# Optimization experiments

Hardware: AMD Instinct MI355X
Metric: run time of the kernel (lower is better)

Reference implementation:

```python
import jax, jax.numpy as jnp
import numpy as np

EPS = 1e-5

def _rmsnorm(x, eps=1e-6):
    # non-affine RMSNorm over last dim (BitNet SubLN-style pre-quant norm)
    return x * jax.lax.rsqrt(jnp.mean(x * x, axis=-1, keepdims=True) + eps)

def _act_quant(x):
    # per-token int8 absmax quantization
    scale = 127.0 / jnp.clip(jnp.max(jnp.abs(x), axis=-1, keepdims=True), EPS)
    return jnp.clip(jnp.round(x * scale), -128, 127) / scale

def _weight_quant(w):
    # per-tensor ternary (1.58-bit) quantization
    scale = 1.0 / jnp.clip(jnp.mean(jnp.abs(w)), EPS)
    return jnp.clip(jnp.round(w * scale), -1, 1) / scale

def _ste(a, q):
    # straight-through estimator: forward = q, backward grad flows to a
    return a + jax.lax.stop_gradient(q - a)

def _bitlinear(x, w):
    # x: [..., in_features], w: [out_features, in_features], no bias
    xn = _rmsnorm(x)
    xq = _ste(xn, _act_quant(xn))
    wq = _ste(w, _weight_quant(w))
    return jnp.einsum('bsd,hd->bsh', xq, wq)


def setup_inputs() -> dict:
    key = jax.random.key(0)
    k_x, k1, k2, k3 = jax.random.split(key, 4)
    B, S, D, H = 4, 4096, 2048, 5632  # hidden = 256*ceil(2048*8/3 / 256)
    return {
        'x': jax.random.normal(k_x, (B, S, D), dtype=jnp.float32),
        'w1': jax.random.normal(k1, (H, D), dtype=jnp.float32) * 0.02,
        'w2': jax.random.normal(k2, (H, D), dtype=jnp.float32) * 0.02,
        'w3': jax.random.normal(k3, (D, H), dtype=jnp.float32) * 0.02,
    }


def reference(x, w1, w2, w3):
    gate = jax.nn.silu(_bitlinear(x, w1))
    up = _bitlinear(x, w2)
    return _bitlinear(gate * up, w3)
```

## Files before the change

kernel.cpp:

```cpp
#include <hip/hip_runtime.h>

typedef int i32x4 __attribute__((ext_vector_type(4)));

static constexpr int M_TOK = 16384;
static constexpr int D_IN  = 2048;
static constexpr int H_FF  = 5632;
static constexpr int NW    = H_FF * D_IN;

__device__ __forceinline__ void async16(const void* g, void* l) {
    __builtin_amdgcn_global_load_lds((__attribute__((address_space(1))) void*)g,
                                     (__attribute__((address_space(3))) void*)l,
                                     16, 0, 0);
}

__device__ __forceinline__ void sbar() {
    asm volatile("" ::: "memory");
    __builtin_amdgcn_s_barrier();
    asm volatile("" ::: "memory");
}
#define WAIT_LGKM(n) { asm volatile("s_waitcnt lgkmcnt(" #n ")" ::: "memory"); \
                       __builtin_amdgcn_sched_barrier(0); }
#define WAIT_VM(n)   { asm volatile("s_waitcnt vmcnt(" #n ")" ::: "memory"); }

__global__ void absum_partial(const float4* __restrict__ w, int n4, double* __restrict__ part) {
    __shared__ double s[256];
    const int t = threadIdx.x;
    double acc = 0.0;
    for (int i = blockIdx.x * 256 + t; i < n4; i += gridDim.x * 256) {
        float4 v = w[i];
        acc += fabs((double)v.x) + fabs((double)v.y) + fabs((double)v.z) + fabs((double)v.w);
    }
    s[t] = acc;
    __syncthreads();
    for (int o = 128; o > 0; o >>= 1) {
        if (t < o) s[t] += s[t + o];
        __syncthreads();
    }
    if (t == 0) part[blockIdx.x] = s[0];
}

__global__ void finalize_scales(const double* __restrict__ parts, double* __restrict__ scales,
                                int nblocks, double inv_n) {
    const int t = threadIdx.x;
    if (t < 3) {
        const double* p = parts + t * nblocks;
        double s = 0.0;
        for (int i = 0; i < nblocks; ++i) s += p[i];
        double c = fmax(s * inv_n, 1e-5);
        scales[t * 2]     = 1.0 / c;
        scales[t * 2 + 1] = c;
    }
}

__global__ void quant_w_kernel(const float4* __restrict__ w, unsigned int* __restrict__ tw,
                               const double* __restrict__ scales, int idx, int n4) {
    const double s = scales[idx * 2];
    const int stride = gridDim.x * blockDim.x;
    for (int i = blockIdx.x * blockDim.x + threadIdx.x; i < n4; i += stride) {
        float4 v = w[i];
        int q0 = (int)fmin(fmax(rint((double)v.x * s), -1.0), 1.0);
        int q1 = (int)fmin(fmax(rint((double)v.y * s), -1.0), 1.0);
        int q2 = (int)fmin(fmax(rint((double)v.z * s), -1.0), 1.0);
        int q3 = (int)fmin(fmax(rint((double)v.w * s), -1.0), 1.0);
        tw[i] = (unsigned int)((q0 & 255) | ((q1 & 255) << 8) |
                               ((q2 & 255) << 16) | ((q3 & 255) << 24));
    }
}

__global__ void quant_x_kernel(const float* __restrict__ x, signed char* __restrict__ qx,
                               double* __restrict__ cx) {
    __shared__ double ssum[256];
    __shared__ float  smax[256];
    const int token = blockIdx.x;
    const int t = threadIdx.x;
    const float4* xr = (const float4*)(x + (size_t)token * D_IN);
    float4 v0 = xr[t];
    float4 v1 = xr[t + 256];
    double ss = (double)v0.x*v0.x + (double)v0.y*v0.y + (double)v0.z*v0.z + (double)v0.w*v0.w
              + (double)v1.x*v1.x + (double)v1.y*v1.y + (double)v1.z*v1.z + (double)v1.w*v1.w;
    float mx = fmaxf(fmaxf(fmaxf(fabsf(v0.x), fabsf(v0.y)), fmaxf(fabsf(v0.z), fabsf(v0.w))),
                     fmaxf(fmaxf(fabsf(v1.x), fabsf(v1.y)), fmaxf(fabsf(v1.z), fabsf(v1.w))));
    ssum[t] = ss; smax[t] = mx;
    __syncthreads();
    for (int o = 128; o > 0; o >>= 1) {
        if (t < o) { ssum[t] += ssum[t + o]; smax[t] = fmaxf(smax[t], smax[t + o]); }
        __syncthreads();
    }
    const double ms    = ssum[0] * (1.0 / (double)D_IN);
    const double r     = 1.0 / sqrt(ms + 1e-6);
    const double den   = fmax((double)smax[0] * r, 1e-5);
    const double scale = 127.0 / den;
    if (t == 0) cx[token] = den * (1.0 / 127.0);

    int q0 = (int)fmin(fmax(rint(((double)v0.x * r) * scale), -128.0), 127.0);
    int q1 = (int)fmin(fmax(rint(((double)v0.y * r) * scale), -128.0), 127.0);
    int q2 = (int)fmin(fmax(rint(((double)v0.z * r) * scale), -128.0), 127.0);
    int q3 = (int)fmin(fmax(rint(((double)v0.w * r) * scale), -128.0), 127.0);
    int q4 = (int)fmin(fmax(rint(((double)v1.x * r) * scale), -128.0), 127.0);
    int q5 = (int)fmin(fmax(rint(((double)v1.y * r) * scale), -128.0), 127.0);
    int q6 = (int)fmin(fmax(rint(((double)v1.z * r) * scale), -128.0), 127.0);
    int q7 = (int)fmin(fmax(rint(((double)v1.w * r) * scale), -128.0), 127.0);
    unsigned int* qr = (unsigned int*)(qx + (size_t)token * D_IN);
    qr[t]       = (unsigned int)((q0 & 255) | ((q1 & 255) << 8) | ((q2 & 255) << 16) | ((q3 & 255) << 24));
    qr[t + 256] = (unsigned int)((q4 & 255) | ((q5 & 255) << 8) | ((q6 & 255) << 16) | ((q7 & 255) << 24));
}

__global__ void quant_h_kernel(float* __restrict__ h, double* __restrict__ ch) {
    __shared__ double ssum[256];
    __shared__ float  smax[256];
    const int token = blockIdx.x;
    const int t = threadIdx.x;
    float* hr = h + (size_t)token * H_FF;
    const float2* h2 = (const float2*)hr;
    float2 vals[11];
    double ss = 0.0;
    float mx = 0.f;
#pragma unroll
    for (int k = 0; k < 11; ++k) {
        float2 v = h2[t + 256 * k];
        vals[k] = v;
        ss += (double)v.x * (double)v.x + (double)v.y * (double)v.y;
        mx = fmaxf(mx, fmaxf(fabsf(v.x), fabsf(v.y)));
    }
    ssum[t] = ss; smax[t] = mx;
    __syncthreads();
    for (int o = 128; o > 0; o >>= 1) {
        if (t < o) { ssum[t] += ssum[t + o]; smax[t] = fmaxf(smax[t], smax[t + o]); }
        __syncthreads();
    }
    const double ms    = ssum[0] * (1.0 / (double)H_FF);
    const double r     = 1.0 / sqrt(ms + 1e-6);
    const double den   = fmax((double)smax[0] * r, 1e-5);
    const double scale = 127.0 / den;
    if (t == 0) ch[token] = den * (1.0 / 127.0);
    unsigned short* qr = (unsigned short*)hr;
#pragma unroll
    for (int k = 0; k < 11; ++k) {
        int a = (int)fmin(fmax(rint(((double)vals[k].x * r) * scale), -128.0), 127.0);
        int b = (int)fmin(fmax(rint(((double)vals[k].y * r) * scale), -128.0), 127.0);
        qr[t + 256 * k] = (unsigned short)((a & 255) | ((b & 255) << 8));
    }
}


__global__ void __launch_bounds__(512, 2) gemm12_kernel(
    const signed char* __restrict__ qx,
    const signed char* __restrict__ tw1,
    const signed char* __restrict__ tw2,
    const double* __restrict__ cx,
    const double* __restrict__ scales,
    float* __restrict__ h)
{
    __shared__ __attribute__((aligned(16))) signed char lds[4][32768];

    const int t = threadIdx.x;
    const int swz = (blockIdx.x & 7) * 352 + (blockIdx.x >> 3);
    const int bm  = swz & 63;
    const int bn  = swz >> 6;

    const int srow = t >> 2;
    const int scol = (((t & 3) ^ ((t >> 3) & 3)) << 4);
    const signed char* gA  = qx  + (size_t)(bm * 256 + srow) * D_IN + scol;
    const signed char* gB1 = tw1 + (size_t)(bn * 128 + srow) * D_IN + scol;
    const signed char* gB2 = tw2 + (size_t)(bn * 128 + srow) * D_IN + scol;
    const size_t arstep = (size_t)128 * D_IN;
    const int l16 = t * 16;

    const int lane = t & 63;
    const int wv = t >> 6;
    const int wm = wv & 3;
    const int wn = wv >> 2;
    const int lm = lane & 15;
    const int kg = lane >> 4;
    const int koff = ((kg ^ ((lm >> 1) & 3)) << 4);

    int aoff[4], boff[4];
#pragma unroll
    for (int i = 0; i < 4; ++i) aoff[i] = (wm * 64 + i * 16 + lm) * 64 + koff;
#pragma unroll
    for (int j = 0; j < 4; ++j) boff[j] = (wn * 64 + j * 16 + lm) * 64 + koff;

    const i32x4 izero = {0, 0, 0, 0};
    i32x4 acc1[4][4], acc2[4][4];
#pragma unroll
    for (int i = 0; i < 4; ++i)
#pragma unroll
        for (int j = 0; j < 4; ++j) { acc1[i][j] = izero; acc2[i][j] = izero; }

    constexpr int NT = D_IN / 64;

#define STAGE12(buf, kt) { const int go = (kt) * 64;                         \
        async16(gA + go,          &lds[buf][l16]);                           \
        async16(gA + arstep + go, &lds[buf][l16 + 8192]);                    \
        async16(gB1 + go, &lds[buf][16384 + l16]);                           \
        async16(gB2 + go, &lds[buf][24576 + l16]); }

    STAGE12(0, 0); STAGE12(1, 1); STAGE12(2, 2);
    WAIT_VM(8);
    sbar();

    for (int kt = 0; kt < NT; ++kt) {
        const int cur = kt & 3;

        i32x4 a[4], b1[4], b2[4];
#pragma unroll
        for (int i = 0; i < 4; ++i) a[i] = *(const i32x4*)&lds[cur][aoff[i]];
#pragma unroll
        for (int j = 0; j < 4; ++j) b1[j] = *(const i32x4*)&lds[cur][16384 + boff[j]];
        __builtin_amdgcn_sched_barrier(0);
#pragma unroll
        for (int j = 0; j < 4; ++j) b2[j] = *(const i32x4*)&lds[cur][24576 + boff[j]];
        __builtin_amdgcn_sched_barrier(0);
        if (kt + 3 < NT) STAGE12((kt + 3) & 3, kt + 3);

        WAIT_LGKM(4);
        __builtin_amdgcn_s_setprio(1);
#pragma unroll
        for (int i = 0; i < 4; ++i)
#pragma unroll
            for (int j = 0; j < 4; ++j)
                acc1[i][j] = __builtin_amdgcn_mfma_i32_16x16x64_i8(a[i], b1[j], acc1[i][j], 0, 0, 0);
        __builtin_amdgcn_s_setprio(0);
        WAIT_LGKM(0);
        __builtin_amdgcn_s_setprio(1);
#pragma unroll
        for (int i = 0; i < 4; ++i)
#pragma unroll
            for (int j = 0; j < 4; ++j)
                acc2[i][j] = __builtin_amdgcn_mfma_i32_16x16x64_i8(a[i], b2[j], acc2[i][j], 0, 0, 0);
        __builtin_amdgcn_s_setprio(0);

        if (kt + 3 < NT)      { WAIT_VM(8); }
        else if (kt + 2 < NT) { WAIT_VM(4); }
        else if (kt + 1 < NT) { WAIT_VM(0); }
        sbar();
    }
#undef STAGE12

    const double cw1 = scales[1];
    const double cw2 = scales[3];
#pragma unroll
    for (int i = 0; i < 4; ++i) {
#pragma unroll
        for (int v = 0; v < 4; ++v) {
            const int row = bm * 256 + wm * 64 + i * 16 + kg * 4 + v;
            const double c  = cx[row];
            const double s1 = c * cw1, s2 = c * cw2;
            float* hp = h + (size_t)row * H_FF + bn * 128 + wn * 64 + lm;
#pragma unroll
            for (int j = 0; j < 4; ++j) {
                float g  = (float)((double)acc1[i][j][v] * s1);
                float u  = (float)((double)acc2[i][j][v] * s2);
                float sg = g / (1.0f + expf(-g));
                hp[j * 16] = sg * u;
            }
        }
    }
}

__global__ void __launch_bounds__(512, 2) gemm3_kernel(
    const signed char* __restrict__ qh,
    const signed char* __restrict__ tw3,
    const double* __restrict__ ch,
    const double* __restrict__ scales,
    float* __restrict__ out)
{
    __shared__ __attribute__((aligned(16))) signed char lds[4][32768];

    const int t = threadIdx.x;
    const int swz = (blockIdx.x & 7) * 64 + (blockIdx.x >> 3);
    const int bm  = swz & 63;
    const int bn  = swz >> 6;

    const int srow = t >> 2;
    const int scol = (((t & 3) ^ ((t >> 3) & 3)) << 4);
    const size_t qh_stride = (size_t)4 * H_FF;
    const signed char* gA = qh  + (size_t)(bm * 256 + srow) * qh_stride + scol;
    const signed char* gB = tw3 + (size_t)(bn * 256 + srow) * H_FF + scol;
    const size_t arstep = (size_t)128 * qh_stride;
    const size_t brstep = (size_t)128 * H_FF;
    const int l16 = t * 16;

    const int lane = t & 63;
    const int wv = t >> 6;
    const int wm = wv >> 2;
    const int wn = wv & 3;
    const int lm = lane & 15;
    const int kg = lane >> 4;
    const int koff = ((kg ^ ((lm >> 1) & 3)) << 4);

    int aoff[8], boff[4];
#pragma unroll
    for (int i = 0; i < 8; ++i) aoff[i] = (wm * 128 + i * 16 + lm) * 64 + koff;
#pragma unroll
    for (int j = 0; j < 4; ++j) boff[j] = (wn * 64 + j * 16 + lm) * 64 + koff;

    const i32x4 izero = {0, 0, 0, 0};
    i32x4 acc[8][4];
#pragma unroll
    for (int i = 0; i < 8; ++i)
#pragma unroll
        for (int j = 0; j < 4; ++j) acc[i][j] = izero;

    constexpr int NT = H_FF / 64;

#define STAGE3(buf, kt) { const int go = (kt) * 64;                          \
        async16(gA + go,          &lds[buf][l16]);                           \
        async16(gA + arstep + go, &lds[buf][l16 + 8192]);                    \
        async16(gB + go,          &lds[buf][16384 + l16]);                   \
        async16(gB + brstep + go, &lds[buf][24576 + l16]); }

    STAGE3(0, 0); STAGE3(1, 1); STAGE3(2, 2);
    WAIT_VM(8);
    sbar();

    for (int kt = 0; kt < NT; ++kt) {
        const int cur = kt & 3;

        i32x4 a[4], b[4], a2[4];
#pragma unroll
        for (int i = 0; i < 4; ++i) a[i] = *(const i32x4*)&lds[cur][aoff[i]];
#pragma unroll
        for (int j = 0; j < 4; ++j) b[j] = *(const i32x4*)&lds[cur][16384 + boff[j]];
        __builtin_amdgcn_sched_barrier(0);
#pragma unroll
        for (int i = 0; i < 4; ++i) a2[i] = *(const i32x4*)&lds[cur][aoff[i + 4]];
        __builtin_amdgcn_sched_barrier(0);
        if (kt + 3 < NT) STAGE3((kt + 3) & 3, kt + 3);

        WAIT_LGKM(4);
        __builtin_amdgcn_s_setprio(1);
#pragma unroll
        for (int i = 0; i < 4; ++i)
#pragma unroll
            for (int j = 0; j < 4; ++j)
                acc[i][j] = __builtin_amdgcn_mfma_i32_16x16x64_i8(a[i], b[j], acc[i][j], 0, 0, 0);
        __builtin_amdgcn_s_setprio(0);
        WAIT_LGKM(0);
        __builtin_amdgcn_s_setprio(1);
#pragma unroll
        for (int i = 0; i < 4; ++i)
#pragma unroll
            for (int j = 0; j < 4; ++j)
                acc[i + 4][j] = __builtin_amdgcn_mfma_i32_16x16x64_i8(a2[i], b[j], acc[i + 4][j], 0, 0, 0);
        __builtin_amdgcn_s_setprio(0);

        if (kt + 3 < NT)      { WAIT_VM(8); }
        else if (kt + 2 < NT) { WAIT_VM(4); }
        else if (kt + 1 < NT) { WAIT_VM(0); }
        sbar();
    }
#undef STAGE3

    const double cw3 = scales[5];
#pragma unroll
    for (int i = 0; i < 8; ++i) {
#pragma unroll
        for (int v = 0; v < 4; ++v) {
            const int row = bm * 256 + wm * 128 + i * 16 + kg * 4 + v;
            const double sc = ch[row] * cw3;
            float* op = out + (size_t)row * D_IN + bn * 256 + wn * 64 + lm;
#pragma unroll
            for (int j = 0; j < 4; ++j) op[j * 16] = (float)((double)acc[i][j][v] * sc);
        }
    }
}

extern "C" void kernel_launch(void* const* d_in, const int* in_sizes, int n_in,
                              void* d_out, int out_size, void* d_ws, size_t ws_size,
                              hipStream_t stream) {
    const float* x  = (const float*)d_in[0];
    const float* w1 = (const float*)d_in[1];
    const float* w2 = (const float*)d_in[2];
    const float* w3 = (const float*)d_in[3];

    char* ws = (char*)d_ws;
    double*      scales = (double*)(ws + 0);
    double*      parts  = (double*)(ws + 256);
    double*      cx     = (double*)(ws + 25088);
    double*      ch     = (double*)(ws + 156416);
    signed char* tw1    = (signed char*)(ws + 287744);
    signed char* tw2    = (signed char*)(ws + 11822336);
    signed char* tw3    = (signed char*)(ws + 23356928);
    float*       hb     = (float*)(ws + 34891520);
    signed char* qx     = (signed char*)(ws + 403990528);

    absum_partial<<<1024, 256, 0, stream>>>((const float4*)w1, NW / 4, parts);
    absum_partial<<<1024, 256, 0, stream>>>((const float4*)w2, NW / 4, parts + 1024);
    absum_partial<<<1024, 256, 0, stream>>>((const float4*)w3, NW / 4, parts + 2048);
    finalize_scales<<<1, 64, 0, stream>>>(parts, scales, 1024, 1.0 / (double)NW);
    quant_w_kernel<<<2048, 256, 0, stream>>>((const float4*)w1, (unsigned int*)tw1, scales, 0, NW / 4);
    quant_w_kernel<<<2048, 256, 0, stream>>>((const float4*)w2, (unsigned int*)tw2, scales, 1, NW / 4);
    quant_w_kernel<<<2048, 256, 0, stream>>>((const float4*)w3, (unsigned int*)tw3, scales, 2, NW / 4);
    quant_x_kernel<<<M_TOK, 256, 0, stream>>>(x, qx, cx);
    gemm12_kernel<<<2816, 512, 0, stream>>>(qx, tw1, tw2, cx, scales, hb);
    quant_h_kernel<<<M_TOK, 256, 0, stream>>>(hb, ch);
    gemm3_kernel<<<512, 512, 0, stream>>>((const signed char*)hb, tw3, ch, scales, (float*)d_out);
}
```

Baseline: 1.100 ms.

## Register double-buffer LDS fragments with 3-stage ring and remap block tile order

Both int8 GEMM kernels now prefetch the next K-tile's LDS fragments into a second register set while MFMAs run on the current set. The shared-memory ring drops from four stages to three, with one barrier per tile placed before staging. The block-to-tile mapping is changed from M-major to N-major grouping for L2 reuse. tw2 is now addressed as tw1+NW, with the workspace offsets moved so the two arrays are contiguous. This is meant to hide LDS read latency behind MFMA work, at the cost of extra VGPRs for the doubled fragment registers, which could hurt occupancy.

```diff
diff --git a/kernel.cpp b/kernel.cpp
--- a/kernel.cpp
+++ b/kernel.cpp
@@ -146,23 +146,21 @@
 __global__ void __launch_bounds__(512, 2) gemm12_kernel(
     const signed char* __restrict__ qx,
     const signed char* __restrict__ tw1,
-    const signed char* __restrict__ tw2,
     const double* __restrict__ cx,
     const double* __restrict__ scales,
     float* __restrict__ h)
 {
-    __shared__ __attribute__((aligned(16))) signed char lds[4][32768];
+    __shared__ __attribute__((aligned(16))) signed char lds[3][32768];
 
     const int t = threadIdx.x;
     const int swz = (blockIdx.x & 7) * 352 + (blockIdx.x >> 3);
-    const int bm  = swz & 63;
-    const int bn  = swz >> 6;
+    const int bm  = swz / 44;
+    const int bn  = swz % 44;
 
     const int srow = t >> 2;
     const int scol = (((t & 3) ^ ((t >> 3) & 3)) << 4);
     const signed char* gA  = qx  + (size_t)(bm * 256 + srow) * D_IN + scol;
     const signed char* gB1 = tw1 + (size_t)(bn * 128 + srow) * D_IN + scol;
-    const signed char* gB2 = tw2 + (size_t)(bn * 128 + srow) * D_IN + scol;
     const size_t arstep = (size_t)128 * D_IN;
     const int l16 = t * 16;
 
@@ -172,13 +170,9 @@
     const int wn = wv >> 2;
     const int lm = lane & 15;
     const int kg = lane >> 4;
-    const int koff = ((kg ^ ((lm >> 1) & 3)) << 4);
-
-    int aoff[4], boff[4];
-#pragma unroll
-    for (int i = 0; i < 4; ++i) aoff[i] = (wm * 64 + i * 16 + lm) * 64 + koff;
-#pragma unroll
-    for (int j = 0; j < 4; ++j) boff[j] = (wn * 64 + j * 16 + lm) * 64 + koff;
+    const int koff  = ((kg ^ ((lm >> 1) & 3)) << 4);
+    const int abase = (wm * 64 + lm) * 64 + koff;
+    const int bbase = (wn * 64 + lm) * 64 + koff;
 
     const i32x4 izero = {0, 0, 0, 0};
     i32x4 acc1[4][4], acc2[4][4];
@@ -187,55 +181,53 @@
 #pragma unroll
         for (int j = 0; j < 4; ++j) { acc1[i][j] = izero; acc2[i][j] = izero; }
 
+    i32x4 fA[12], fB[12];
+
     constexpr int NT = D_IN / 64;
 
 #define STAGE12(buf, kt) { const int go = (kt) * 64;                         \
-        async16(gA + go,          &lds[buf][l16]);                           \
-        async16(gA + arstep + go, &lds[buf][l16 + 8192]);                    \
-        async16(gB1 + go, &lds[buf][16384 + l16]);                           \
-        async16(gB2 + go, &lds[buf][24576 + l16]); }
+        async16(gA + go,           &lds[buf][l16]);                          \
+        async16(gA + arstep + go,  &lds[buf][l16 + 8192]);                   \
+        async16(gB1 + go,          &lds[buf][16384 + l16]);                  \
+        async16(gB1 + NW + go,     &lds[buf][24576 + l16]); }
+#define LOADF12(R, buf) {                                                    \
+        _Pragma("unroll") for (int i = 0; i < 4; ++i)                        \
+            R[i]     = *(const i32x4*)&lds[buf][abase + i * 1024];           \
+        _Pragma("unroll") for (int j = 0; j < 4; ++j)                        \
+            R[4 + j] = *(const i32x4*)&lds[buf][16384 + bbase + j * 1024];   \
+        _Pragma("unroll") for (int j = 0; j < 4; ++j)                        \
+            R[8 + j] = *(const i32x4*)&lds[buf][24576 + bbase + j * 1024]; }
+#define MFMAS12(R) {                                                         \
+        __builtin_amdgcn_s_setprio(1);                                       \
+        _Pragma("unroll") for (int i = 0; i < 4; ++i)                        \
+        _Pragma("unroll") for (int j = 0; j < 4; ++j)                        \
+            acc1[i][j] = __builtin_amdgcn_mfma_i32_16x16x64_i8(R[i], R[4 + j], acc1[i][j], 0, 0, 0); \
+        _Pragma("unroll") for (int i = 0; i < 4; ++i)                        \
+        _Pragma("unroll") for (int j = 0; j < 4; ++j)                        \
+            acc2[i][j] = __builtin_amdgcn_mfma_i32_16x16x64_i8(R[i], R[8 + j], acc2[i][j], 0, 0, 0); \
+        __builtin_amdgcn_s_setprio(0); }
+#define TILE12(kt, RCUR, RNXT) {                                             \
+        if ((kt) + 2 < NT) { WAIT_VM(4); } else { WAIT_VM(0); }              \
+        sbar();                                                              \
+        if ((kt) + 3 < NT) STAGE12(((kt) % 3), (kt) + 3);                    \
+        if ((kt) + 1 < NT) LOADF12(RNXT, (((kt) + 1) % 3));                  \
+        __builtin_amdgcn_sched_barrier(0);                                   \
+        MFMAS12(RCUR);                                                       \
+        WAIT_LGKM(0); }
 
     STAGE12(0, 0); STAGE12(1, 1); STAGE12(2, 2);
-    WAIT_VM(8);
-    sbar();
-
-    for (int kt = 0; kt < NT; ++kt) {
-        const int cur = kt & 3;
-
-        i32x4 a[4], b1[4], b2[4];
-#pragma unroll
-        for (int i = 0; i < 4; ++i) a[i] = *(const i32x4*)&lds[cur][aoff[i]];
-#pragma unroll
-        for (int j = 0; j < 4; ++j) b1[j] = *(const i32x4*)&lds[cur][16384 + boff[j]];
-        __builtin_amdgcn_sched_barrier(0);
-#pragma unroll
-        for (int j = 0; j < 4; ++j) b2[j] = *(const i32x4*)&lds[cur][24576 + boff[j]];
-        __builtin_amdgcn_sched_barrier(0);
-        if (kt + 3 < NT) STAGE12((kt + 3) & 3, kt + 3);
-
-        WAIT_LGKM(4);
-        __builtin_amdgcn_s_setprio(1);
-#pragma unroll
-        for (int i = 0; i < 4; ++i)
-#pragma unroll
-            for (int j = 0; j < 4; ++j)
-                acc1[i][j] = __builtin_amdgcn_mfma_i32_16x16x64_i8(a[i], b1[j], acc1[i][j], 0, 0, 0);
-        __builtin_amdgcn_s_setprio(0);
-        WAIT_LGKM(0);
-        __builtin_amdgcn_s_setprio(1);
-#pragma unroll
-        for (int i = 0; i < 4; ++i)
-#pragma unroll
-            for (int j = 0; j < 4; ++j)
-                acc2[i][j] = __builtin_amdgcn_mfma_i32_16x16x64_i8(a[i], b2[j], acc2[i][j], 0, 0, 0);
-        __builtin_amdgcn_s_setprio(0);
-
-        if (kt + 3 < NT)      { WAIT_VM(8); }
-        else if (kt + 2 < NT) { WAIT_VM(4); }
-        else if (kt + 1 < NT) { WAIT_VM(0); }
-        sbar();
+    WAIT_VM(8); sbar();
+    LOADF12(fA, 0);
+    WAIT_LGKM(0);
+
+    for (int kt = 0; kt < NT; kt += 2) {
+        TILE12(kt,     fA, fB);
+        TILE12(kt + 1, fB, fA);
     }
 #undef STAGE12
+#undef LOADF12
+#undef MFMAS12
+#undef TILE12
 
     const double cw1 = scales[1];
     const double cw2 = scales[3];
@@ -265,12 +257,12 @@
     const double* __restrict__ scales,
     float* __restrict__ out)
 {
-    __shared__ __attribute__((aligned(16))) signed char lds[4][32768];
+    __shared__ __attribute__((aligned(16))) signed char lds[3][32768];
 
     const int t = threadIdx.x;
     const int swz = (blockIdx.x & 7) * 64 + (blockIdx.x >> 3);
-    const int bm  = swz & 63;
-    const int bn  = swz >> 6;
+    const int bm  = swz >> 3;
+    const int bn  = swz & 7;
 
     const int srow = t >> 2;
     const int scol = (((t & 3) ^ ((t >> 3) & 3)) << 4);
@@ -287,13 +279,9 @@
     const int wn = wv & 3;
     const int lm = lane & 15;
     const int kg = lane >> 4;
-    const int koff = ((kg ^ ((lm >> 1) & 3)) << 4);
-
-    int aoff[8], boff[4];
-#pragma unroll
-    for (int i = 0; i < 8; ++i) aoff[i] = (wm * 128 + i * 16 + lm) * 64 + koff;
-#pragma unroll
-    for (int j = 0; j < 4; ++j) boff[j] = (wn * 64 + j * 16 + lm) * 64 + koff;
+    const int koff  = ((kg ^ ((lm >> 1) & 3)) << 4);
+    const int abase = (wm * 128 + lm) * 64 + koff;
+    const int bbase = (wn * 64 + lm) * 64 + koff;
 
     const i32x4 izero = {0, 0, 0, 0};
     i32x4 acc[8][4];
@@ -301,6 +289,8 @@
     for (int i = 0; i < 8; ++i)
 #pragma unroll
         for (int j = 0; j < 4; ++j) acc[i][j] = izero;
+
+    i32x4 fA[12], fB[12];
 
     constexpr int NT = H_FF / 64;
 
@@ -309,48 +299,44 @@
         async16(gA + arstep + go, &lds[buf][l16 + 8192]);                    \
         async16(gB + go,          &lds[buf][16384 + l16]);                   \
         async16(gB + brstep + go, &lds[buf][24576 + l16]); }
+#define LOADF3(R, buf) {                                                     \
+        _Pragma("unroll") for (int i = 0; i < 4; ++i)                        \
+            R[i]     = *(const i32x4*)&lds[buf][abase + i * 1024];           \
+        _Pragma("unroll") for (int j = 0; j < 4; ++j)                        \
+            R[4 + j] = *(const i32x4*)&lds[buf][16384 + bbase + j * 1024];   \
+        _Pragma("unroll") for (int i = 0; i < 4; ++i)                        \
+            R[8 + i] = *(const i32x4*)&lds[buf][abase + 4096 + i * 1024]; }
+#define MFMAS3(R) {                                                          \
+        __builtin_amdgcn_s_setprio(1);                                       \
+        _Pragma("unroll") for (int i = 0; i < 4; ++i)                        \
+        _Pragma("unroll") for (int j = 0; j < 4; ++j)                        \
+            acc[i][j] = __builtin_amdgcn_mfma_i32_16x16x64_i8(R[i], R[4 + j], acc[i][j], 0, 0, 0); \
+        _Pragma("unroll") for (int i = 0; i < 4; ++i)                        \
+        _Pragma("unroll") for (int j = 0; j < 4; ++j)                        \
+            acc[4 + i][j] = __builtin_amdgcn_mfma_i32_16x16x64_i8(R[8 + i], R[4 + j], acc[4 + i][j], 0, 0, 0); \
+        __builtin_amdgcn_s_setprio(0); }
+#define TILE3(kt, RCUR, RNXT) {                                              \
+        if ((kt) + 2 < NT) { WAIT_VM(4); } else { WAIT_VM(0); }              \
+        sbar();                                                              \
+        if ((kt) + 3 < NT) STAGE3(((kt) % 3), (kt) + 3);                     \
+        if ((kt) + 1 < NT) LOADF3(RNXT, (((kt) + 1) % 3));                   \
+        __builtin_amdgcn_sched_barrier(0);                                   \
+        MFMAS3(RCUR);                                                        \
+        WAIT_LGKM(0); }
 
     STAGE3(0, 0); STAGE3(1, 1); STAGE3(2, 2);
-    WAIT_VM(8);
-    sbar();
-
-    for (int kt = 0; kt < NT; ++kt) {
-        const int cur = kt & 3;
-
-        i32x4 a[4], b[4], a2[4];
-#pragma unroll
-        for (int i = 0; i < 4; ++i) a[i] = *(const i32x4*)&lds[cur][aoff[i]];
-#pragma unroll
-        for (int j = 0; j < 4; ++j) b[j] = *(const i32x4*)&lds[cur][16384 + boff[j]];
-        __builtin_amdgcn_sched_barrier(0);
-#pragma unroll
-        for (int i = 0; i < 4; ++i) a2[i] = *(const i32x4*)&lds[cur][aoff[i + 4]];
-        __builtin_amdgcn_sched_barrier(0);
-        if (kt + 3 < NT) STAGE3((kt + 3) & 3, kt + 3);
-
-        WAIT_LGKM(4);
-        __builtin_amdgcn_s_setprio(1);
-#pragma unroll
-        for (int i = 0; i < 4; ++i)
-#pragma unroll
-            for (int j = 0; j < 4; ++j)
-                acc[i][j] = __builtin_amdgcn_mfma_i32_16x16x64_i8(a[i], b[j], acc[i][j], 0, 0, 0);
-        __builtin_amdgcn_s_setprio(0);
-        WAIT_LGKM(0);
-        __builtin_amdgcn_s_setprio(1);
-#pragma unroll
-        for (int i = 0; i < 4; ++i)
-#pragma unroll
-            for (int j = 0; j < 4; ++j)
-                acc[i + 4][j] = __builtin_amdgcn_mfma_i32_16x16x64_i8(a2[i], b[j], acc[i + 4][j], 0, 0, 0);
-        __builtin_amdgcn_s_setprio(0);
-
-        if (kt + 3 < NT)      { WAIT_VM(8); }
-        else if (kt + 2 < NT) { WAIT_VM(4); }
-        else if (kt + 1 < NT) { WAIT_VM(0); }
-        sbar();
+    WAIT_VM(8); sbar();
+    LOADF3(fA, 0);
+    WAIT_LGKM(0);
+
+    for (int kt = 0; kt < NT; kt += 2) {
+        TILE3(kt,     fA, fB);
+        TILE3(kt + 1, fB, fA);
     }
 #undef STAGE3
+#undef LOADF3
+#undef MFMAS3
+#undef TILE3
 
     const double cw3 = scales[5];
 #pragma unroll
@@ -380,8 +366,8 @@
     double*      cx     = (double*)(ws + 25088);
     double*      ch     = (double*)(ws + 156416);
     signed char* tw1    = (signed char*)(ws + 287744);
-    signed char* tw2    = (signed char*)(ws + 11822336);
-    signed char* tw3    = (signed char*)(ws + 23356928);
+    signed char* tw2    = (signed char*)(ws + 11822080);
+    signed char* tw3    = (signed char*)(ws + 23356416);
     float*       hb     = (float*)(ws + 34891520);
     signed char* qx     = (signed char*)(ws + 403990528);
 
@@ -393,7 +379,7 @@
     quant_w_kernel<<<2048, 256, 0, stream>>>((const float4*)w2, (unsigned int*)tw2, scales, 1, NW / 4);
     quant_w_kernel<<<2048, 256, 0, stream>>>((const float4*)w3, (unsigned int*)tw3, scales, 2, NW / 4);
     quant_x_kernel<<<M_TOK, 256, 0, stream>>>(x, qx, cx);
-    gemm12_kernel<<<2816, 512, 0, stream>>>(qx, tw1, tw2, cx, scales, hb);
+    gemm12_kernel<<<2816, 512, 0, stream>>>(qx, tw1, cx, scales, hb);
     quant_h_kernel<<<M_TOK, 256, 0, stream>>>(hb, ch);
     gemm3_kernel<<<512, 512, 0, stream>>>((const signed char*)hb, tw3, ch, scales, (float*)d_out);
 }
```

Result: faster. 1.077 ms (-2.1%).

## Shrink GEMM tiles and LDS buffering to raise occupancy to four blocks per CU

Applied to the files above, without the earlier changes.

Both int8 GEMMs move to smaller N tiles (64 columns per weight for gate/up, 128 for the down projection) and from four LDS stages to two, which cuts LDS use to 48KB and halves the accumulators so launch bounds can ask for four blocks per CU. The gate and up weights are now packed contiguously so a single B pointer loads both halves, and the tw2/tw3 workspace offsets change to match. Grid sizes double. The aim is more resident waves to hide latency, at the cost of a shallower prefetch pipeline with a full vmcnt(0) wait every iteration and less data reuse per tile, which means more reads of A.

```diff
diff --git a/kernel.cpp b/kernel.cpp
--- a/kernel.cpp
+++ b/kernel.cpp
@@ -143,27 +143,27 @@
 }
 
 
-__global__ void __launch_bounds__(512, 2) gemm12_kernel(
+__global__ void __launch_bounds__(512, 4) gemm12_kernel(
     const signed char* __restrict__ qx,
     const signed char* __restrict__ tw1,
-    const signed char* __restrict__ tw2,
     const double* __restrict__ cx,
     const double* __restrict__ scales,
     float* __restrict__ h)
 {
-    __shared__ __attribute__((aligned(16))) signed char lds[4][32768];
-
-    const int t = threadIdx.x;
-    const int swz = (blockIdx.x & 7) * 352 + (blockIdx.x >> 3);
-    const int bm  = swz & 63;
-    const int bn  = swz >> 6;
+    __shared__ __attribute__((aligned(16))) signed char lds[2][24576];
+
+    const int t = threadIdx.x;
+    const int swz = (blockIdx.x & 7) * 704 + (blockIdx.x >> 3);
+    const int bm  = swz / 88;
+    const int bn  = swz % 88;
 
     const int srow = t >> 2;
     const int scol = (((t & 3) ^ ((t >> 3) & 3)) << 4);
-    const signed char* gA  = qx  + (size_t)(bm * 256 + srow) * D_IN + scol;
-    const signed char* gB1 = tw1 + (size_t)(bn * 128 + srow) * D_IN + scol;
-    const signed char* gB2 = tw2 + (size_t)(bn * 128 + srow) * D_IN + scol;
+    const signed char* gA = qx + (size_t)(bm * 256 + srow) * D_IN + scol;
     const size_t arstep = (size_t)128 * D_IN;
+    const int brow = srow & 63;
+    const signed char* gB = tw1 + (srow >= 64 ? (size_t)NW : (size_t)0)
+                                + (size_t)(bn * 64 + brow) * D_IN + scol;
     const int l16 = t * 16;
 
     const int lane = t & 63;
@@ -172,53 +172,46 @@
     const int wn = wv >> 2;
     const int lm = lane & 15;
     const int kg = lane >> 4;
-    const int koff = ((kg ^ ((lm >> 1) & 3)) << 4);
-
-    int aoff[4], boff[4];
-#pragma unroll
-    for (int i = 0; i < 4; ++i) aoff[i] = (wm * 64 + i * 16 + lm) * 64 + koff;
-#pragma unroll
-    for (int j = 0; j < 4; ++j) boff[j] = (wn * 64 + j * 16 + lm) * 64 + koff;
+    const int koff  = ((kg ^ ((lm >> 1) & 3)) << 4);
+    const int abase = (wm * 64 + lm) * 64 + koff;
+    const int bbase = 16384 + (wn * 32 + lm) * 64 + koff;
 
     const i32x4 izero = {0, 0, 0, 0};
-    i32x4 acc1[4][4], acc2[4][4];
+    i32x4 acc1[4][2], acc2[4][2];
 #pragma unroll
     for (int i = 0; i < 4; ++i)
 #pragma unroll
-        for (int j = 0; j < 4; ++j) { acc1[i][j] = izero; acc2[i][j] = izero; }
+        for (int j = 0; j < 2; ++j) { acc1[i][j] = izero; acc2[i][j] = izero; }
 
     constexpr int NT = D_IN / 64;
 
 #define STAGE12(buf, kt) { const int go = (kt) * 64;                         \
         async16(gA + go,          &lds[buf][l16]);                           \
-        async16(gA + arstep + go, &lds[buf][l16 + 8192]);                    \
-        async16(gB1 + go, &lds[buf][16384 + l16]);                           \
-        async16(gB2 + go, &lds[buf][24576 + l16]); }
-
-    STAGE12(0, 0); STAGE12(1, 1); STAGE12(2, 2);
-    WAIT_VM(8);
-    sbar();
+        async16(gA + arstep + go, &lds[buf][8192 + l16]);                    \
+        async16(gB + go,          &lds[buf][16384 + l16]); }
+
+    STAGE12(0, 0);
+    WAIT_VM(0); sbar();
 
     for (int kt = 0; kt < NT; ++kt) {
-        const int cur = kt & 3;
-
-        i32x4 a[4], b1[4], b2[4];
-#pragma unroll
-        for (int i = 0; i < 4; ++i) a[i] = *(const i32x4*)&lds[cur][aoff[i]];
-#pragma unroll
-        for (int j = 0; j < 4; ++j) b1[j] = *(const i32x4*)&lds[cur][16384 + boff[j]];
+        const int cur = kt & 1;
+        if (kt + 1 < NT) STAGE12(cur ^ 1, kt + 1);
+
+        i32x4 a[4], b1[2], b2[2];
+#pragma unroll
+        for (int i = 0; i < 4; ++i) a[i] = *(const i32x4*)&lds[cur][abase + i * 1024];
+#pragma unroll
+        for (int j = 0; j < 2; ++j) b1[j] = *(const i32x4*)&lds[cur][bbase + j * 1024];
         __builtin_amdgcn_sched_barrier(0);
 #pragma unroll
-        for (int j = 0; j < 4; ++j) b2[j] = *(const i32x4*)&lds[cur][24576 + boff[j]];
-        __builtin_amdgcn_sched_barrier(0);
-        if (kt + 3 < NT) STAGE12((kt + 3) & 3, kt + 3);
-
-        WAIT_LGKM(4);
+        for (int j = 0; j < 2; ++j) b2[j] = *(const i32x4*)&lds[cur][bbase + 4096 + j * 1024];
+
+        WAIT_LGKM(2);
         __builtin_amdgcn_s_setprio(1);
 #pragma unroll
         for (int i = 0; i < 4; ++i)
 #pragma unroll
-            for (int j = 0; j < 4; ++j)
+            for (int j = 0; j < 2; ++j)
                 acc1[i][j] = __builtin_amdgcn_mfma_i32_16x16x64_i8(a[i], b1[j], acc1[i][j], 0, 0, 0);
         __builtin_amdgcn_s_setprio(0);
         WAIT_LGKM(0);
@@ -226,13 +219,11 @@
 #pragma unroll
         for (int i = 0; i < 4; ++i)
 #pragma unroll
-            for (int j = 0; j < 4; ++j)
+            for (int j = 0; j < 2; ++j)
                 acc2[i][j] = __builtin_amdgcn_mfma_i32_16x16x64_i8(a[i], b2[j], acc2[i][j], 0, 0, 0);
         __builtin_amdgcn_s_setprio(0);
 
-        if (kt + 3 < NT)      { WAIT_VM(8); }
-        else if (kt + 2 < NT) { WAIT_VM(4); }
-        else if (kt + 1 < NT) { WAIT_VM(0); }
+        WAIT_VM(0);
         sbar();
     }
 #undef STAGE12
@@ -246,9 +237,9 @@
             const int row = bm * 256 + wm * 64 + i * 16 + kg * 4 + v;
             const double c  = cx[row];
             const double s1 = c * cw1, s2 = c * cw2;
-            float* hp = h + (size_t)row * H_FF + bn * 128 + wn * 64 + lm;
-#pragma unroll
-            for (int j = 0; j < 4; ++j) {
+            float* hp = h + (size_t)row * H_FF + bn * 64 + wn * 32 + lm;
+#pragma unroll
+            for (int j = 0; j < 2; ++j) {
                 float g  = (float)((double)acc1[i][j][v] * s1);
                 float u  = (float)((double)acc2[i][j][v] * s2);
                 float sg = g / (1.0f + expf(-g));
@@ -258,47 +249,42 @@
     }
 }
 
-__global__ void __launch_bounds__(512, 2) gemm3_kernel(
+__global__ void __launch_bounds__(512, 4) gemm3_kernel(
     const signed char* __restrict__ qh,
     const signed char* __restrict__ tw3,
     const double* __restrict__ ch,
     const double* __restrict__ scales,
     float* __restrict__ out)
 {
-    __shared__ __attribute__((aligned(16))) signed char lds[4][32768];
-
-    const int t = threadIdx.x;
-    const int swz = (blockIdx.x & 7) * 64 + (blockIdx.x >> 3);
-    const int bm  = swz & 63;
-    const int bn  = swz >> 6;
+    __shared__ __attribute__((aligned(16))) signed char lds[2][24576];
+
+    const int t = threadIdx.x;
+    const int swz = (blockIdx.x & 7) * 128 + (blockIdx.x >> 3);
+    const int bm  = swz >> 4;
+    const int bn  = swz & 15;
 
     const int srow = t >> 2;
     const int scol = (((t & 3) ^ ((t >> 3) & 3)) << 4);
     const size_t qh_stride = (size_t)4 * H_FF;
     const signed char* gA = qh  + (size_t)(bm * 256 + srow) * qh_stride + scol;
-    const signed char* gB = tw3 + (size_t)(bn * 256 + srow) * H_FF + scol;
+    const signed char* gB = tw3 + (size_t)(bn * 128 + srow) * H_FF + scol;
     const size_t arstep = (size_t)128 * qh_stride;
-    const size_t brstep = (size_t)128 * H_FF;
     const int l16 = t * 16;
 
     const int lane = t & 63;
     const int wv = t >> 6;
-    const int wm = wv >> 2;
-    const int wn = wv & 3;
+    const int wm = wv & 3;
+    const int wn = wv >> 2;
     const int lm = lane & 15;
     const int kg = lane >> 4;
-    const int koff = ((kg ^ ((lm >> 1) & 3)) << 4);
-
-    int aoff[8], boff[4];
-#pragma unroll
-    for (int i = 0; i < 8; ++i) aoff[i] = (wm * 128 + i * 16 + lm) * 64 + koff;
-#pragma unroll
-    for (int j = 0; j < 4; ++j) boff[j] = (wn * 64 + j * 16 + lm) * 64 + koff;
+    const int koff  = ((kg ^ ((lm >> 1) & 3)) << 4);
+    const int abase = (wm * 64 + lm) * 64 + koff;
+    const int bbase = 16384 + (wn * 64 + lm) * 64 + koff;
 
     const i32x4 izero = {0, 0, 0, 0};
-    i32x4 acc[8][4];
-#pragma unroll
-    for (int i = 0; i < 8; ++i)
+    i32x4 acc[4][4];
+#pragma unroll
+    for (int i = 0; i < 4; ++i)
 #pragma unroll
         for (int j = 0; j < 4; ++j) acc[i][j] = izero;
 
@@ -306,34 +292,31 @@
 
 #define STAGE3(buf, kt) { const int go = (kt) * 64;                          \
         async16(gA + go,          &lds[buf][l16]);                           \
-        async16(gA + arstep + go, &lds[buf][l16 + 8192]);                    \
-        async16(gB + go,          &lds[buf][16384 + l16]);                   \
-        async16(gB + brstep + go, &lds[buf][24576 + l16]); }
-
-    STAGE3(0, 0); STAGE3(1, 1); STAGE3(2, 2);
-    WAIT_VM(8);
-    sbar();
+        async16(gA + arstep + go, &lds[buf][8192 + l16]);                    \
+        async16(gB + go,          &lds[buf][16384 + l16]); }
+
+    STAGE3(0, 0);
+    WAIT_VM(0); sbar();
 
     for (int kt = 0; kt < NT; ++kt) {
-        const int cur = kt & 3;
-
-        i32x4 a[4], b[4], a2[4];
-#pragma unroll
-        for (int i = 0; i < 4; ++i) a[i] = *(const i32x4*)&lds[cur][aoff[i]];
-#pragma unroll
-        for (int j = 0; j < 4; ++j) b[j] = *(const i32x4*)&lds[cur][16384 + boff[j]];
+        const int cur = kt & 1;
+        if (kt + 1 < NT) STAGE3(cur ^ 1, kt + 1);
+
+        i32x4 a[4], b[4];
+#pragma unroll
+        for (int i = 0; i < 4; ++i) a[i] = *(const i32x4*)&lds[cur][abase + i * 1024];
+#pragma unroll
+        for (int j = 0; j < 2; ++j) b[j] = *(const i32x4*)&lds[cur][bbase + j * 1024];
         __builtin_amdgcn_sched_barrier(0);
 #pragma unroll
-        for (int i = 0; i < 4; ++i) a2[i] = *(const i32x4*)&lds[cur][aoff[i + 4]];
-        __builtin_amdgcn_sched_barrier(0);
-        if (kt + 3 < NT) STAGE3((kt + 3) & 3, kt + 3);
-
-        WAIT_LGKM(4);
+        for (int j = 2; j < 4; ++j) b[j] = *(const i32x4*)&lds[cur][bbase + j * 1024];
+
+        WAIT_LGKM(2);
         __builtin_amdgcn_s_setprio(1);
 #pragma unroll
         for (int i = 0; i < 4; ++i)
 #pragma unroll
-            for (int j = 0; j < 4; ++j)
+            for (int j = 0; j < 2; ++j)
                 acc[i][j] = __builtin_amdgcn_mfma_i32_16x16x64_i8(a[i], b[j], acc[i][j], 0, 0, 0);
         __builtin_amdgcn_s_setprio(0);
         WAIT_LGKM(0);
@@ -341,25 +324,23 @@
 #pragma unroll
         for (int i = 0; i < 4; ++i)
 #pragma unroll
-            for (int j = 0; j < 4; ++j)
-                acc[i + 4][j] = __builtin_amdgcn_mfma_i32_16x16x64_i8(a2[i], b[j], acc[i + 4][j], 0, 0, 0);
+            for (int j = 2; j < 4; ++j)
+                acc[i][j] = __builtin_amdgcn_mfma_i32_16x16x64_i8(a[i], b[j], acc[i][j], 0, 0, 0);
         __builtin_amdgcn_s_setprio(0);
 
-        if (kt + 3 < NT)      { WAIT_VM(8); }
-        else if (kt + 2 < NT) { WAIT_VM(4); }
-        else if (kt + 1 < NT) { WAIT_VM(0); }
+        WAIT_VM(0);
         sbar();
     }
 #undef STAGE3
 
     const double cw3 = scales[5];
 #pragma unroll
-    for (int i = 0; i < 8; ++i) {
+    for (int i = 0; i < 4; ++i) {
 #pragma unroll
         for (int v = 0; v < 4; ++v) {
-            const int row = bm * 256 + wm * 128 + i * 16 + kg * 4 + v;
+            const int row = bm * 256 + wm * 64 + i * 16 + kg * 4 + v;
             const double sc = ch[row] * cw3;
-            float* op = out + (size_t)row * D_IN + bn * 256 + wn * 64 + lm;
+            float* op = out + (size_t)row * D_IN + bn * 128 + wn * 64 + lm;
 #pragma unroll
             for (int j = 0; j < 4; ++j) op[j * 16] = (float)((double)acc[i][j][v] * sc);
         }
@@ -380,8 +361,8 @@
     double*      cx     = (double*)(ws + 25088);
     double*      ch     = (double*)(ws + 156416);
     signed char* tw1    = (signed char*)(ws + 287744);
-    signed char* tw2    = (signed char*)(ws + 11822336);
-    signed char* tw3    = (signed char*)(ws + 23356928);
+    signed char* tw2    = (signed char*)(ws + 11822080);
+    signed char* tw3    = (signed char*)(ws + 23356416);
     float*       hb     = (float*)(ws + 34891520);
     signed char* qx     = (signed char*)(ws + 403990528);
 
@@ -393,7 +374,7 @@
     quant_w_kernel<<<2048, 256, 0, stream>>>((const float4*)w2, (unsigned int*)tw2, scales, 1, NW / 4);
     quant_w_kernel<<<2048, 256, 0, stream>>>((const float4*)w3, (unsigned int*)tw3, scales, 2, NW / 4);
     quant_x_kernel<<<M_TOK, 256, 0, stream>>>(x, qx, cx);
-    gemm12_kernel<<<2816, 512, 0, stream>>>(qx, tw1, tw2, cx, scales, hb);
+    gemm12_kernel<<<5632, 512, 0, stream>>>(qx, tw1, cx, scales, hb);
     quant_h_kernel<<<M_TOK, 256, 0, stream>>>(hb, ch);
-    gemm3_kernel<<<512, 512, 0, stream>>>((const signed char*)hb, tw3, ch, scales, (float*)d_out);
-}
+    gemm3_kernel<<<1024, 512, 0, stream>>>((const signed char*)hb, tw3, ch, scales, (float*)d_out);
+}
```

Measured after the change: 1.095 ms. No clear change (-0.5%).
